# Kernel tuning notes

Hardware: AMD Instinct MI355X
Metric: run time of the kernel (lower is better)

The kernel has to match this reference:

```python
import jax, jax.numpy as jnp
import numpy as np

B, T, N, H, E, R = 512, 10, 50, 200, 10000, 200

def _aggregate(neigh, neigh_len, hist_len, ids, rids, ent, rel, Wa, ba, v):
    # neigh: [B,T,N] entity ids; returns padded GRU input [B,T,3H]
    h = Wa.shape[0]
    e = ent[neigh]                                  # [B,T,N,h] neighbor embeds
    se = ent[ids]                                   # [B,h]
    re_a = ent[rids]                                # faithful: original uses ent_embeds[r] in attention
    Wn, Ws, Wr = Wa[:, :h], Wa[:, h:2 * h], Wa[:, 2 * h:]
    pre = jnp.einsum('btnh,gh->btng', e, Wn) + (se @ Ws.T + re_a @ Wr.T + ba)[:, None, None, :]
    logits = (jnp.tanh(pre) @ v)[..., 0]            # [B,T,N]
    nmask = jnp.arange(neigh.shape[2])[None, None, :] < neigh_len[:, :, None]
    logits = jnp.where(nmask, logits, -1e30)
    w = jax.nn.softmax(logits, axis=-1)             # per-timestep softmax over valid neighbors
    step = jnp.einsum('btn,btnh->bth', w, e)        # attention-pooled neighbor embed
    rr = rel[rids]                                  # rel_embeds used in the GRU-input concat
    seq = jnp.concatenate([step,
                           jnp.broadcast_to(se[:, None, :], step.shape),
                           jnp.broadcast_to(rr[:, None, :], step.shape)], axis=-1)
    smask = jnp.arange(neigh.shape[1])[None, :] < hist_len[:, None]
    return seq * smask[..., None]                   # zeros past each sample's history length

def _gru(seq, lengths, Wih, Whh, bih, bhh):
    # packed_padded GRU equivalent: hidden freezes at each sample's true length
    Bb, Tt, _ = seq.shape
    h = Whh.shape[1]
    mask = jnp.arange(Tt)[None, :] < lengths[:, None]
    def step(hprev, xm):
        x, m = xm
        gi = x @ Wih.T + bih
        gh = hprev @ Whh.T + bhh
        ir, iz, inn = jnp.split(gi, 3, axis=-1)
        hr, hz, hn = jnp.split(gh, 3, axis=-1)
        rg = jax.nn.sigmoid(ir + hr)
        zg = jax.nn.sigmoid(iz + hz)
        ng = jnp.tanh(inn + rg * hn)
        hnew = (1.0 - zg) * ng + zg * hprev
        return jnp.where(m[:, None], hnew, hprev), None
    h0 = jnp.zeros((Bb, h), seq.dtype)
    hf, _ = jax.lax.scan(step, h0, (seq.transpose(1, 0, 2), mask.T))
    return hf

def _ce(logits, labels):
    lp = jax.nn.log_softmax(logits, axis=-1)
    return -jnp.mean(jnp.take_along_axis(lp, labels[:, None], axis=-1)[:, 0])

def setup_inputs() -> dict:
    key = jax.random.key(0)
    ks = jax.random.split(key, 32)
    d = {}
    d['triplets'] = jnp.stack([jax.random.randint(ks[0], (B,), 0, E),
                               jax.random.randint(ks[1], (B,), 0, R),
                               jax.random.randint(ks[2], (B,), 0, E)], axis=1)
    d['s_hist_neigh'] = jax.random.randint(ks[3], (B, T, N), 0, E)
    d['s_neigh_len'] = jax.random.randint(ks[4], (B, T), 1, N + 1)
    d['s_hist_len'] = jax.random.randint(ks[5], (B,), 1, T + 1)
    d['o_hist_neigh'] = jax.random.randint(ks[6], (B, T, N), 0, E)
    d['o_neigh_len'] = jax.random.randint(ks[7], (B, T), 1, N + 1)
    d['o_hist_len'] = jax.random.randint(ks[8], (B,), 1, T + 1)
    sc = 0.05
    d['ent_embeds'] = jax.random.normal(ks[9], (E, H)) * sc
    d['rel_embeds'] = jax.random.normal(ks[10], (R, H)) * sc
    d['attn_s_w'] = jax.random.normal(ks[11], (H, 3 * H)) * sc
    d['attn_s_b'] = jnp.zeros((H,))
    d['v_s'] = jax.random.normal(ks[12], (H, 1)) * sc
    d['attn_o_w'] = jax.random.normal(ks[13], (H, 3 * H)) * sc
    d['attn_o_b'] = jnp.zeros((H,))
    d['v_o'] = jax.random.normal(ks[14], (H, 1)) * sc
    d['sub_w_ih'] = jax.random.normal(ks[15], (3 * H, 3 * H)) * sc
    d['sub_w_hh'] = jax.random.normal(ks[16], (3 * H, H)) * sc
    d['sub_b_ih'] = jnp.zeros((3 * H,))
    d['sub_b_hh'] = jnp.zeros((3 * H,))
    d['ob_w_ih'] = jax.random.normal(ks[17], (3 * H, 3 * H)) * sc
    d['ob_w_hh'] = jax.random.normal(ks[18], (3 * H, H)) * sc
    d['ob_b_ih'] = jnp.zeros((3 * H,))
    d['ob_b_hh'] = jnp.zeros((3 * H,))
    d['lin_sub_w'] = jax.random.normal(ks[19], (E, 3 * H)) * sc
    d['lin_sub_b'] = jnp.zeros((E,))
    d['lin_ob_w'] = jax.random.normal(ks[20], (E, 3 * H)) * sc
    d['lin_ob_b'] = jnp.zeros((E,))
    return d

def reference(triplets, s_hist_neigh, s_neigh_len, s_hist_len, o_hist_neigh, o_neigh_len, o_hist_len,
              ent_embeds, rel_embeds, attn_s_w, attn_s_b, v_s, attn_o_w, attn_o_b, v_o,
              sub_w_ih, sub_w_hh, sub_b_ih, sub_b_hh, ob_w_ih, ob_w_hh, ob_b_ih, ob_b_hh,
              lin_sub_w, lin_sub_b, lin_ob_w, lin_ob_b):
    s, r, o = triplets[:, 0], triplets[:, 1], triplets[:, 2]
    s_idx = jnp.argsort(-s_hist_len)   # descending sort by history length
    o_idx = jnp.argsort(-o_hist_len)
    seq_s = _aggregate(s_hist_neigh, s_neigh_len, s_hist_len, s, r, ent_embeds, rel_embeds, attn_s_w, attn_s_b, v_s)
    seq_o = _aggregate(o_hist_neigh, o_neigh_len, o_hist_len, o, r, ent_embeds, rel_embeds, attn_o_w, attn_o_b, v_o)
    s_h = _gru(seq_s, s_hist_len, sub_w_ih, sub_w_hh, sub_b_ih, sub_b_hh)[s_idx]
    o_h = _gru(seq_o, o_hist_len, ob_w_ih, ob_w_hh, ob_b_ih, ob_b_hh)[o_idx]
    ob_pred = jnp.concatenate([ent_embeds[s[s_idx]], s_h, rel_embeds[r[s_idx]]], axis=1) @ lin_sub_w.T + lin_sub_b
    sub_pred = jnp.concatenate([ent_embeds[o[o_idx]], o_h, rel_embeds[r[o_idx]]], axis=1) @ lin_ob_w.T + lin_ob_b
    loss = _ce(ob_pred, o[s_idx]) + _ce(sub_pred, s[o_idx])
    return loss, sub_pred, ob_pred, o_idx, s_idx
```

## Files before the change

### kernel.cpp

```cpp
#include <hip/hip_runtime.h>
#include <hip/hip_bf16.h>
#include <math.h>

typedef __hip_bfloat16 bf16;
typedef __attribute__((ext_vector_type(8))) short short8;
typedef __attribute__((ext_vector_type(4))) float f32x4;

#define B_ 512
#define T_ 10
#define N_ 50
#define H_ 200
#define E_ 10000
#define R_ 200
#define K3 600

__device__ __forceinline__ float b2f(bf16 x){ return __bfloat162float(x); }
__device__ __forceinline__ float u2f(unsigned short u){
  unsigned int x = ((unsigned int)u) << 16;
  return __builtin_bit_cast(float, x);
}
__device__ __forceinline__ float fsigm(float x){
  return __builtin_amdgcn_rcpf(1.f + __expf(-x));
}
__device__ __forceinline__ float ftanh(float x){
  x = fminf(15.f, fmaxf(-15.f, x));
  float e = __expf(-2.f * x);
  return (1.f - e) * __builtin_amdgcn_rcpf(1.f + e);
}

__global__ void k_init(float* lossacc){ if(threadIdx.x < 4) lossacc[threadIdx.x] = 0.f; }

__global__ __launch_bounds__(256) void k_pack_wn(
    const float* __restrict__ Wa0, const float* __restrict__ Wa1, bf16* __restrict__ Wn2)
{
  int r = blockIdx.x;
  const float* Wa = (r < 200) ? Wa0 : Wa1;
  int g = (r < 200) ? r : r - 200;
  bf16* out = Wn2 + (size_t)r * 256;
  for (int k = threadIdx.x; k < 256; k += 256) {
    float v = (r < 400 && k < 200) ? Wa[(size_t)g * K3 + k] : 0.f;
    out[k] = __float2bfloat16(v);
  }
}

__global__ __launch_bounds__(256) void k_pack_w400(
    const float* __restrict__ W0, const float* __restrict__ W1,
    bf16* __restrict__ dst, int nrows, int rpad)
{
  int r = blockIdx.x, side = blockIdx.y;
  const float* W = side ? W1 : W0;
  bf16* out = dst + ((size_t)side * rpad + r) * 448;
  for (int k = threadIdx.x; k < 448; k += 256) {
    float v = (r < nrows && k < 400) ? W[(size_t)r * K3 + 200 + k] : 0.f;
    out[k] = __float2bfloat16(v);
  }
}

__global__ __launch_bounds__(256) void k_pack_wstep(
    const float* __restrict__ W0, const float* __restrict__ W1, bf16* __restrict__ dst)
{
  int r = blockIdx.x, side = blockIdx.y;
  const float* W = side ? W1 : W0;
  bf16* out = dst + ((size_t)side * 640 + r) * 256;
  for (int k = threadIdx.x; k < 256; k += 256) {
    float v = (r < 600 && k < 200) ? W[(size_t)r * K3 + k] : 0.f;
    out[k] = __float2bfloat16(v);
  }
}

__global__ __launch_bounds__(256) void k_pack_whh(
    const float* __restrict__ W0, const float* __restrict__ W1, bf16* __restrict__ dst)
{
  int r = blockIdx.x, side = blockIdx.y;
  const float* W = side ? W1 : W0;
  bf16* out = dst + ((size_t)side * 608 + r) * 224;
  for (int k = threadIdx.x; k < 224; k += 256) {
    float v = (r < 600 && k < 200) ? W[(size_t)r * H_ + k] : 0.f;
    out[k] = __float2bfloat16(v);
  }
}

__global__ __launch_bounds__(256) void k_afeats(
    const float* __restrict__ ent, const float* __restrict__ rel, const int* __restrict__ trip,
    bf16* __restrict__ Ab, bf16* __restrict__ Ag)
{
  int b = blockIdx.x, side = blockIdx.y;
  int ids = trip[b * 3 + (side ? 2 : 0)];
  int rid = trip[b * 3 + 1];
  size_t ro = ((size_t)side * B_ + b) * 448;
  for (int k = threadIdx.x; k < 448; k += 256) {
    float vb = 0.f, vg = 0.f;
    if (k < 200) { float e = ent[(size_t)ids * H_ + k]; vb = e; vg = e; }
    else if (k < 400) {
      vb = ent[(size_t)rid * H_ + (k - 200)];
      vg = rel[(size_t)rid * H_ + (k - 200)];
    }
    Ab[ro + k] = __float2bfloat16(vb);
    Ag[ro + k] = __float2bfloat16(vg);
  }
}

template<bool OUTBF, bool AF32>
__global__ __launch_bounds__(256) void k_gg(
    const void* __restrict__ Aptr, const bf16* __restrict__ Bptr,
    const float* __restrict__ bias0, const float* __restrict__ bias1,
    void* __restrict__ Cptr,
    int M, int Nout, int KP, int Acols,
    long Astride, long Bstride, long Cstride, int Nstride)
{
  int side = blockIdx.z;
  int m0 = blockIdx.x * 128, n0 = blockIdx.y * 64;

  __shared__ bf16 As[128][72];
  __shared__ bf16 Bs[64][72];

  int tid = threadIdx.x;
  int wave = tid >> 6, lane = tid & 63;
  int quad = lane >> 4, l15 = lane & 15;

  f32x4 acc[8];
  #pragma unroll
  for (int mt = 0; mt < 8; mt++) acc[mt] = (f32x4){0,0,0,0};

  int arow = tid >> 1, ac0 = (tid & 1) * 32;
  int gr = m0 + arow; if (gr > M - 1) gr = M - 1;
  int brow = tid >> 2, bc0 = (tid & 3) * 16;

  for (int k0 = 0; k0 < KP; k0 += 64) {
    if (AF32) {
      const float* src = (const float*)Aptr + (size_t)gr * Acols;
      #pragma unroll
      for (int u = 0; u < 8; u++) {
        int kk = k0 + ac0 + u * 4;
        float4 v;
        if (kk + 4 <= Acols) v = *(const float4*)&src[kk];
        else {
          v.x = (kk + 0 < Acols) ? src[kk + 0] : 0.f;
          v.y = (kk + 1 < Acols) ? src[kk + 1] : 0.f;
          v.z = (kk + 2 < Acols) ? src[kk + 2] : 0.f;
          v.w = (kk + 3 < Acols) ? src[kk + 3] : 0.f;
        }
        As[arow][ac0 + u * 4 + 0] = __float2bfloat16(v.x);
        As[arow][ac0 + u * 4 + 1] = __float2bfloat16(v.y);
        As[arow][ac0 + u * 4 + 2] = __float2bfloat16(v.z);
        As[arow][ac0 + u * 4 + 3] = __float2bfloat16(v.w);
      }
    } else {
      const bf16* src = (const bf16*)Aptr + (size_t)side * Astride + (size_t)gr * KP + k0 + ac0;
      #pragma unroll
      for (int u = 0; u < 4; u++)
        *(short8*)&As[arow][ac0 + u * 8] = *(const short8*)&src[u * 8];
    }
    {
      const bf16* src = Bptr + (size_t)side * Bstride + (size_t)(n0 + brow) * KP + k0 + bc0;
      *(short8*)&Bs[brow][bc0]     = *(const short8*)&src[0];
      *(short8*)&Bs[brow][bc0 + 8] = *(const short8*)&src[8];
    }
    __syncthreads();
    #pragma unroll
    for (int ks = 0; ks < 2; ks++) {
      int kk = ks * 32 + quad * 8;
      short8 bfr = *(const short8*)&Bs[wave * 16 + l15][kk];
      #pragma unroll
      for (int mt = 0; mt < 8; mt++) {
        short8 afr = *(const short8*)&As[mt * 16 + l15][kk];
        acc[mt] = __builtin_amdgcn_mfma_f32_16x16x32_bf16(afr, bfr, acc[mt], 0, 0, 0);
      }
    }
    __syncthreads();
  }

  int n = n0 + wave * 16 + l15;
  if (n < Nout) {
    float bv = bias0 ? (side ? bias1[n] : bias0[n]) : 0.f;
    #pragma unroll
    for (int mt = 0; mt < 8; mt++) {
      #pragma unroll
      for (int r = 0; r < 4; r++) {
        int m = m0 + mt * 16 + quad * 4 + r;
        if (m < M) {
          float val = acc[mt][r] + bv;
          if (OUTBF)
            ((bf16*)Cptr)[(size_t)side * Cstride + (size_t)m * Nstride + n] = __float2bfloat16(val);
          else
            ((float*)Cptr)[(size_t)side * Cstride + (size_t)m * Nstride + n] = val;
        }
      }
    }
  }
}

__global__ __launch_bounds__(256) void k_attn3(
    const float* __restrict__ ent,
    const int* __restrict__ neigh0, const int* __restrict__ neigh1,
    const int* __restrict__ nlen0, const int* __restrict__ nlen1,
    const int* __restrict__ hlen0, const int* __restrict__ hlen1,
    const float* __restrict__ v0, const float* __restrict__ v1,
    const bf16* __restrict__ ep2, const float* __restrict__ biasb,
    bf16* __restrict__ stepb)
{
  int side = blockIdx.y;
  int bt = blockIdx.x;
  int b = bt / T_, t = bt % T_;
  int hl = (side ? hlen1 : hlen0)[b];
  bf16* srow = stepb + (((size_t)side * B_ + b) * T_ + t) * 256;
  int tid = threadIdx.x;
  if (t >= hl) {
    srow[tid] = __float2bfloat16(0.f);
    return;
  }
  const int* neigh = side ? neigh1 : neigh0;
  const float* v = side ? v1 : v0;
  const float* brow = biasb + ((size_t)side * B_ + b) * H_;
  int nl = (side ? nlen1 : nlen0)[b * T_ + t];

  __shared__ float bsh[H_], vsh[H_], lg[64], wsh[64];
  __shared__ int nb[N_];
  if (tid < H_) { bsh[tid] = brow[tid]; vsh[tid] = v[tid]; }
  if (tid < N_) nb[tid] = neigh[((size_t)b * T_ + t) * N_ + tid];
  __syncthreads();

  int grp = tid >> 4;
  int l16 = tid & 15;

  float bs[13], vs[13];
  #pragma unroll
  for (int i = 0; i < 13; i++) {
    int g = l16 + i * 16;
    bool ok = (g < H_);
    bs[i] = ok ? bsh[g] : 0.f;
    vs[i] = ok ? vsh[g] : 0.f;
  }

  for (int n = grp; n < nl; n += 16) {
    const bf16* er = ep2 + (size_t)nb[n] * 400 + side * 200;
    float acc = 0.f;
    #pragma unroll
    for (int i = 0; i < 13; i++) {
      int g = l16 + i * 16;
      float e = (g < H_) ? b2f(er[g]) : 0.f;
      acc += ftanh(e + bs[i]) * vs[i];
    }
    #pragma unroll
    for (int off = 8; off > 0; off >>= 1) acc += __shfl_down(acc, off, 16);
    if (l16 == 0) lg[n] = acc;
  }
  __syncthreads();

  if (tid < 64) {
    float x = (tid < nl) ? lg[tid] : -1e30f;
    float m = x;
    #pragma unroll
    for (int off = 32; off > 0; off >>= 1) m = fmaxf(m, __shfl_down(m, off));
    m = __shfl(m, 0);
    float e = (tid < nl) ? __expf(x - m) : 0.f;
    float s = e;
    #pragma unroll
    for (int off = 32; off > 0; off >>= 1) s += __shfl_down(s, off);
    s = __shfl(s, 0);
    if (tid < N_) wsh[tid] = e / s;
  }
  __syncthreads();

  int h = tid;
  if (h < H_) {
    float a0 = 0.f, a1 = 0.f, a2 = 0.f, a3 = 0.f;
    int n = 0;
    for (; n + 4 <= nl; n += 4) {
      a0 += wsh[n + 0] * ent[(size_t)nb[n + 0] * H_ + h];
      a1 += wsh[n + 1] * ent[(size_t)nb[n + 1] * H_ + h];
      a2 += wsh[n + 2] * ent[(size_t)nb[n + 2] * H_ + h];
      a3 += wsh[n + 3] * ent[(size_t)nb[n + 3] * H_ + h];
    }
    for (; n < nl; n++) a0 += wsh[n] * ent[(size_t)nb[n] * H_ + h];
    srow[h] = __float2bfloat16((a0 + a1) + (a2 + a3));
  } else {
    srow[h] = __float2bfloat16(0.f);
  }
}

__global__ __launch_bounds__(832) void k_gru4(
    const bf16* __restrict__ giall, const bf16* __restrict__ gibase,
    const bf16* __restrict__ Whh2,
    const float* __restrict__ bhh0, const float* __restrict__ bhh1,
    const int* __restrict__ len0, const int* __restrict__ len1,
    float* __restrict__ hfin)
{
  int side = blockIdx.y;
  int b0 = blockIdx.x * 16;
  const bf16* gia = giall + ((size_t)side * B_ * T_ + (size_t)b0 * T_) * 600;
  const bf16* gib = gibase + ((size_t)side * B_ + b0) * K3;
  const bf16* Wh  = Whh2 + (size_t)side * 608 * 224;
  const float* bhh = side ? bhh1 : bhh0;
  const int* len = side ? len1 : len0;

  __shared__ __align__(16) bf16 Hs[2][16][232];

  int tid = threadIdx.x;
  int wave = tid >> 6, lane = tid & 63;
  int quad = lane >> 4, l15 = lane & 15;

  for (int i = tid; i < 2 * 16 * 232 / 8; i += 832) ((short8*)&Hs[0][0][0])[i] = (short8)0;

  int j0 = wave * 16;
  int j = j0 + l15;
  bool jok = (j < H_);
  float bhr = 0.f, bhz = 0.f, bhn = 0.f;
  float gr[4] = {}, gz[4] = {}, gn[4] = {};
  int lens4[4];
  #pragma unroll
  for (int r = 0; r < 4; r++) lens4[r] = len[b0 + quad * 4 + r];
  if (jok) {
    bhr = bhh[j]; bhz = bhh[H_ + j]; bhn = bhh[2 * H_ + j];
    #pragma unroll
    for (int r = 0; r < 4; r++) {
      const bf16* g = gib + (size_t)(quad * 4 + r) * K3;
      gr[r] = b2f(g[j]); gz[r] = b2f(g[H_ + j]); gn[r] = b2f(g[2 * H_ + j]);
    }
  }
  const bf16* wr = Wh + (size_t)j * 224;
  const bf16* wz = Wh + (size_t)(200 + j) * 224;
  const bf16* wn = Wh + (size_t)(400 + j) * 224;
  __syncthreads();

  int cur = 0;
  for (int t = 0; t < T_; t++) {
    unsigned short guR[4], guZ[4], guN[4];
    if (jok) {
      #pragma unroll
      for (int r = 0; r < 4; r++) {
        const unsigned short* g =
            (const unsigned short*)(gia + ((size_t)(quad * 4 + r) * T_ + t) * 600);
        guR[r] = g[j]; guZ[r] = g[200 + j]; guN[r] = g[400 + j];
      }
    }
    f32x4 ar = {0,0,0,0}, az = {0,0,0,0}, anh = {0,0,0,0};
    #pragma unroll
    for (int ks = 0; ks < 7; ks++) {
      int kk = ks * 32 + quad * 8;
      short8 a0 = *(const short8*)&Hs[cur][l15][kk];
      short8 br = *(const short8*)&wr[kk];
      short8 bz = *(const short8*)&wz[kk];
      short8 bn = *(const short8*)&wn[kk];
      ar  = __builtin_amdgcn_mfma_f32_16x16x32_bf16(a0, br, ar, 0, 0, 0);
      az  = __builtin_amdgcn_mfma_f32_16x16x32_bf16(a0, bz, az, 0, 0, 0);
      anh = __builtin_amdgcn_mfma_f32_16x16x32_bf16(a0, bn, anh, 0, 0, 0);
    }
    if (jok) {
      #pragma unroll
      for (int r = 0; r < 4; r++) {
        int row = quad * 4 + r;
        float rz  = ar[r] + u2f(guR[r]) + gr[r] + bhr;
        float zz  = az[r] + u2f(guZ[r]) + gz[r] + bhz;
        float inn = u2f(guN[r]) + gn[r];
        float hn  = anh[r] + bhn;
        float rg = fsigm(rz);
        float zg = fsigm(zz);
        float ng = ftanh(inn + rg * hn);
        float hold = b2f(Hs[cur][row][j]);
        float hnew = (1.f - zg) * ng + zg * hold;
        Hs[cur ^ 1][row][j] = __float2bfloat16((t < lens4[r]) ? hnew : hold);
      }
    }
    __syncthreads();
    cur ^= 1;
  }
  for (int i = tid; i < 16 * H_; i += 832) {
    int row = i / H_, jj = i % H_;
    hfin[((size_t)side * B_ + b0 + row) * H_ + jj] = b2f(Hs[cur][row][jj]);
  }
}

__global__ __launch_bounds__(512) void k_argsort(
    const int* __restrict__ hlen0, const int* __restrict__ hlen1,
    int* __restrict__ idxbuf, float* __restrict__ dout)
{
  int side = blockIdx.x;
  const int* len = side ? hlen1 : hlen0;
  __shared__ int lens[B_];
  __shared__ int perm[B_];
  int tid = threadIdx.x;
  lens[tid] = len[tid];
  __syncthreads();
  int L = lens[tid];
  int rank = 0;
  for (int j = 0; j < B_; j++) {
    int Lj = lens[j];
    rank += (Lj > L) || (Lj == L && j < tid);
  }
  perm[rank] = tid;
  __syncthreads();
  idxbuf[side * B_ + tid] = perm[tid];
  size_t base = 1 + (size_t)2 * B_ * E_ + (side ? 0 : B_);
  dout[base + tid] = (float)perm[tid];
}

__global__ __launch_bounds__(256) void k_feat(
    const float* __restrict__ ent, const float* __restrict__ rel, const int* __restrict__ trip,
    const int* __restrict__ idxbuf, const float* __restrict__ hfin,
    bf16* __restrict__ xfeat)
{
  int i = blockIdx.x, p = blockIdx.y;
  int bi = idxbuf[(p == 0 ? 1 : 0) * B_ + i];
  int ent_id = (p == 0) ? trip[bi * 3 + 2] : trip[bi * 3 + 0];
  int rid = trip[bi * 3 + 1];
  const float* hsrc = hfin + (size_t)(p == 0 ? 1 : 0) * B_ * H_;
  bf16* x = xfeat + ((size_t)p * B_ + i) * 640;
  int h = threadIdx.x;
  if (h < H_) {
    x[h]          = __float2bfloat16(ent[(size_t)ent_id * H_ + h]);
    x[H_ + h]     = __float2bfloat16(hsrc[(size_t)bi * H_ + h]);
    x[2 * H_ + h] = __float2bfloat16(rel[(size_t)rid * H_ + h]);
  }
  if (h < 40) x[600 + h] = __float2bfloat16(0.f);
}

__global__ __launch_bounds__(512) void k_gemm5(
    const bf16* __restrict__ Abf,
    const float* __restrict__ B0, const float* __restrict__ B1,
    const float* __restrict__ bias0, const float* __restrict__ bias1,
    float* __restrict__ dout)
{
  int side = blockIdx.z;
  const float* Bm = side ? B1 : B0;
  const float* bias = side ? bias1 : bias0;
  float* C = dout + 1 + (size_t)side * B_ * E_;
  int mBase = blockIdx.x * 256;
  int m0 = side * B_ + mBase;
  int n0 = blockIdx.y * 64;

  __shared__ bf16 As[256][72];
  __shared__ bf16 Bs[64][72];

  int tid = threadIdx.x;
  int wave = tid >> 6, lane = tid & 63;
  int quad = lane >> 4, l15 = lane & 15;
  int wm = wave >> 1, wn = wave & 1;

  f32x4 acc[4][2];
  #pragma unroll
  for (int mt = 0; mt < 4; mt++)
    #pragma unroll
    for (int nt = 0; nt < 2; nt++) acc[mt][nt] = (f32x4){0,0,0,0};

  int arow = tid >> 1, ac0 = (tid & 1) * 32;
  int brow = tid >> 3, bc0 = (tid & 7) * 8;
  const bf16* asrc = Abf + (size_t)(m0 + arow) * 640 + ac0;
  int nsrc = n0 + brow; if (nsrc > E_ - 1) nsrc = E_ - 1;
  const float* bsrc = Bm + (size_t)nsrc * K3 + bc0;

  for (int k0 = 0; k0 < 640; k0 += 64) {
    #pragma unroll
    for (int u = 0; u < 4; u++)
      *(short8*)&As[arow][ac0 + u * 8] = *(const short8*)&asrc[k0 + u * 8];
    {
      int kb = k0 + bc0;
      if (kb + 8 <= K3) {
        float4 v0 = *(const float4*)&bsrc[k0];
        float4 v1 = *(const float4*)&bsrc[k0 + 4];
        Bs[brow][bc0 + 0] = __float2bfloat16(v0.x);
        Bs[brow][bc0 + 1] = __float2bfloat16(v0.y);
        Bs[brow][bc0 + 2] = __float2bfloat16(v0.z);
        Bs[brow][bc0 + 3] = __float2bfloat16(v0.w);
        Bs[brow][bc0 + 4] = __float2bfloat16(v1.x);
        Bs[brow][bc0 + 5] = __float2bfloat16(v1.y);
        Bs[brow][bc0 + 6] = __float2bfloat16(v1.z);
        Bs[brow][bc0 + 7] = __float2bfloat16(v1.w);
      } else {
        #pragma unroll
        for (int u = 0; u < 8; u++) {
          int k = kb + u;
          float v = (k < K3) ? bsrc[k0 + u] : 0.f;
          Bs[brow][bc0 + u] = __float2bfloat16(v);
        }
      }
    }
    __syncthreads();
    #pragma unroll
    for (int ks = 0; ks < 2; ks++) {
      int kk = ks * 32 + quad * 8;
      short8 bfr[2];
      #pragma unroll
      for (int nt = 0; nt < 2; nt++)
        bfr[nt] = *(const short8*)&Bs[wn * 32 + nt * 16 + l15][kk];
      #pragma unroll
      for (int mt = 0; mt < 4; mt++) {
        short8 afr = *(const short8*)&As[wm * 64 + mt * 16 + l15][kk];
        #pragma unroll
        for (int nt = 0; nt < 2; nt++)
          acc[mt][nt] = __builtin_amdgcn_mfma_f32_16x16x32_bf16(afr, bfr[nt], acc[mt][nt], 0, 0, 0);
      }
    }
    __syncthreads();
  }

  #pragma unroll
  for (int nt = 0; nt < 2; nt++) {
    int n = n0 + wn * 32 + nt * 16 + l15;
    if (n < E_) {
      float bv = bias[n];
      #pragma unroll
      for (int mt = 0; mt < 4; mt++) {
        #pragma unroll
        for (int r = 0; r < 4; r++) {
          int mrow = mBase + wm * 64 + mt * 16 + quad * 4 + r;
          C[(size_t)mrow * E_ + n] = acc[mt][nt][r] + bv;
        }
      }
    }
  }
}

__global__ __launch_bounds__(256) void k_loss(
    const float* __restrict__ dout, const int* __restrict__ trip,
    const int* __restrict__ idxbuf, float* __restrict__ lossacc)
{
  int i = blockIdx.x, p = blockIdx.y;
  const float* row = dout + 1 + (size_t)p * B_ * E_ + (size_t)i * E_;
  int tid = threadIdx.x;
  float m = -1e30f, s = 0.f;
  for (int e = tid; e < E_; e += 256) {
    float x = row[e];
    if (x > m) { s = s * expf(m - x) + 1.f; m = x; }
    else s += expf(x - m);
  }
  __shared__ float ms[256], ss[256];
  ms[tid] = m; ss[tid] = s; __syncthreads();
  for (int st = 128; st > 0; st >>= 1) {
    if (tid < st) {
      float m2 = ms[tid + st], s2 = ss[tid + st];
      float m1 = ms[tid], s1 = ss[tid];
      float mm = fmaxf(m1, m2);
      ss[tid] = s1 * expf(m1 - mm) + s2 * expf(m2 - mm);
      ms[tid] = mm;
    }
    __syncthreads();
  }
  if (tid == 0) {
    int bi = idxbuf[(p == 0 ? 1 : 0) * B_ + i];
    int label = (p == 0) ? trip[bi * 3 + 0] : trip[bi * 3 + 2];
    float lp = row[label] - ms[0] - logf(ss[0]);
    atomicAdd(lossacc, -lp / (float)B_);
  }
}

__global__ void k_loss_write(const float* __restrict__ lossacc, float* __restrict__ dout){
  if (threadIdx.x == 0) dout[0] = lossacc[0];
}

extern "C" void kernel_launch(void* const* d_in, const int* in_sizes, int n_in,
                              void* d_out, int out_size, void* d_ws, size_t ws_size,
                              hipStream_t stream)
{
  const int* trip = (const int*)d_in[0];
  const int* s_ne = (const int*)d_in[1];
  const int* s_nl = (const int*)d_in[2];
  const int* s_hl = (const int*)d_in[3];
  const int* o_ne = (const int*)d_in[4];
  const int* o_nl = (const int*)d_in[5];
  const int* o_hl = (const int*)d_in[6];
  const float* ent = (const float*)d_in[7];
  const float* rel = (const float*)d_in[8];
  const float* aw_s = (const float*)d_in[9];
  const float* ab_s = (const float*)d_in[10];
  const float* v_s  = (const float*)d_in[11];
  const float* aw_o = (const float*)d_in[12];
  const float* ab_o = (const float*)d_in[13];
  const float* v_o  = (const float*)d_in[14];
  const float* sub_wih = (const float*)d_in[15];
  const float* sub_whh = (const float*)d_in[16];
  const float* sub_bih = (const float*)d_in[17];
  const float* sub_bhh = (const float*)d_in[18];
  const float* ob_wih  = (const float*)d_in[19];
  const float* ob_whh  = (const float*)d_in[20];
  const float* ob_bih  = (const float*)d_in[21];
  const float* ob_bhh  = (const float*)d_in[22];
  const float* lin_sub_w = (const float*)d_in[23];
  const float* lin_sub_b = (const float*)d_in[24];
  const float* lin_ob_w  = (const float*)d_in[25];
  const float* lin_ob_b  = (const float*)d_in[26];
  float* dout = (float*)d_out;

  char* w = (char*)d_ws;
  bf16* ep2     = (bf16*)w;  w += (size_t)E_ * 400 * 2;
  bf16* stepb   = (bf16*)w;  w += (size_t)2 * B_ * T_ * 256 * 2;
  float* biasb  = (float*)w; w += (size_t)2 * B_ * H_ * 4;
  bf16* gibase  = (bf16*)w;  w += (size_t)2 * B_ * K3 * 2;
  float* hfin   = (float*)w; w += (size_t)2 * B_ * H_ * 4;
  bf16* xfeat   = (bf16*)w;  w += (size_t)1024 * 640 * 2;
  bf16* Wn2     = (bf16*)w;  w += (size_t)448 * 256 * 2;
  bf16* Wb2     = (bf16*)w;  w += (size_t)2 * 256 * 448 * 2;
  bf16* Wg2     = (bf16*)w;  w += (size_t)2 * 640 * 448 * 2;
  bf16* Wstep   = (bf16*)w;  w += (size_t)2 * 640 * 256 * 2;
  bf16* Whh2    = (bf16*)w;  w += (size_t)2 * 608 * 224 * 2;
  bf16* giall   = (bf16*)w;  w += (size_t)2 * B_ * T_ * 600 * 2;
  bf16* Abias   = (bf16*)w;  w += (size_t)2 * B_ * 448 * 2;
  bf16* Agi     = (bf16*)w;  w += (size_t)2 * B_ * 448 * 2;
  float* lossacc= (float*)w; w += 256;
  int* idxbuf   = (int*)w;   w += 4096;

  k_init<<<1, 64, 0, stream>>>(lossacc);
  k_pack_wn<<<448, 256, 0, stream>>>(aw_s, aw_o, Wn2);
  k_pack_w400<<<dim3(256, 2), 256, 0, stream>>>(aw_s, aw_o, Wb2, 200, 256);
  k_pack_w400<<<dim3(640, 2), 256, 0, stream>>>(sub_wih, ob_wih, Wg2, 600, 640);
  k_pack_wstep<<<dim3(640, 2), 256, 0, stream>>>(sub_wih, ob_wih, Wstep);
  k_pack_whh<<<dim3(608, 2), 256, 0, stream>>>(sub_whh, ob_whh, Whh2);
  k_afeats<<<dim3(B_, 2), 256, 0, stream>>>(ent, rel, trip, Abias, Agi);
  k_gg<true, true><<<dim3(79, 7, 1), 256, 0, stream>>>(
      (const void*)ent, Wn2, nullptr, nullptr, (void*)ep2,
      E_, 400, 256, 200, 0L, 0L, 0L, 400);
  k_gg<false, false><<<dim3(4, 4, 2), 256, 0, stream>>>(
      (const void*)Abias, Wb2, ab_s, ab_o, (void*)biasb,
      B_, 200, 448, 448, (long)B_ * 448, 256L * 448, (long)B_ * 200, 200);
  k_gg<true, false><<<dim3(4, 10, 2), 256, 0, stream>>>(
      (const void*)Agi, Wg2, sub_bih, ob_bih, (void*)gibase,
      B_, 600, 448, 448, (long)B_ * 448, 640L * 448, (long)B_ * 600, 600);
  k_attn3<<<dim3(B_ * T_, 2), 256, 0, stream>>>(ent, s_ne, o_ne, s_nl, o_nl,
                                                s_hl, o_hl, v_s, v_o, ep2, biasb, stepb);
  k_gg<true, false><<<dim3(40, 10, 2), 256, 0, stream>>>(
      (const void*)stepb, Wstep, nullptr, nullptr, (void*)giall,
      B_ * T_, 600, 256, 256, (long)B_ * T_ * 256, 640L * 256, (long)B_ * T_ * 600, 600);
  k_gru4<<<dim3(B_ / 16, 2), 832, 0, stream>>>(giall, gibase, Whh2, sub_bhh, ob_bhh,
                                               s_hl, o_hl, hfin);
  k_argsort<<<2, 512, 0, stream>>>(s_hl, o_hl, idxbuf, dout);
  k_feat<<<dim3(B_, 2), 256, 0, stream>>>(ent, rel, trip, idxbuf, hfin, xfeat);
  k_gemm5<<<dim3(2, (E_ + 63) / 64, 2), 512, 0, stream>>>(
      xfeat, lin_ob_w, lin_sub_w, lin_ob_b, lin_sub_b, dout);
  k_loss<<<dim3(B_, 2), 256, 0, stream>>>(dout, trip, idxbuf, lossacc);
  k_loss_write<<<1, 64, 0, stream>>>(lossacc, dout);
}
```

Baseline: 421.0 us.

## Pre-pack output linear weights to bf16 and merge pack kernels into one launch

Merges the six small packing and init kernels into a single launch, which cuts launch overhead. Adds a kernel that converts the two 10000x600 fp32 output-projection weights into padded bf16 once per call. A new GEMM then reads these bf16 tiles directly instead of converting fp32 to bf16 inside every tile load. The cost is an extra full pass over about 48MB of fp32 weights plus a bf16 write, and the new path only runs if the workspace is large enough.

```diff
diff --git a/kernel.cpp b/kernel.cpp
--- a/kernel.cpp
+++ b/kernel.cpp
@@ -13,6 +13,7 @@
 #define E_ 10000
 #define R_ 200
 #define K3 600
+#define EP_ 10048
 
 __device__ __forceinline__ float b2f(bf16 x){ return __bfloat162float(x); }
 __device__ __forceinline__ float u2f(unsigned short u){
@@ -28,75 +29,93 @@
   return (1.f - e) * __builtin_amdgcn_rcpf(1.f + e);
 }
 
-__global__ void k_init(float* lossacc){ if(threadIdx.x < 4) lossacc[threadIdx.x] = 0.f; }
-
-__global__ __launch_bounds__(256) void k_pack_wn(
-    const float* __restrict__ Wa0, const float* __restrict__ Wa1, bf16* __restrict__ Wn2)
-{
-  int r = blockIdx.x;
-  const float* Wa = (r < 200) ? Wa0 : Wa1;
-  int g = (r < 200) ? r : r - 200;
-  bf16* out = Wn2 + (size_t)r * 256;
-  for (int k = threadIdx.x; k < 256; k += 256) {
-    float v = (r < 400 && k < 200) ? Wa[(size_t)g * K3 + k] : 0.f;
+__global__ __launch_bounds__(256) void k_packall(
+    const float* __restrict__ aw_s, const float* __restrict__ aw_o,
+    const float* __restrict__ sub_wih, const float* __restrict__ ob_wih,
+    const float* __restrict__ sub_whh, const float* __restrict__ ob_whh,
+    const float* __restrict__ ent, const float* __restrict__ rel,
+    const int* __restrict__ trip,
+    bf16* __restrict__ Wn2, bf16* __restrict__ Wb2, bf16* __restrict__ Wg2,
+    bf16* __restrict__ Wstep, bf16* __restrict__ Whh2,
+    bf16* __restrict__ Ab, bf16* __restrict__ Ag, float* __restrict__ lossacc)
+{
+  int bid = blockIdx.x;
+  int tid = threadIdx.x;
+  if (bid < 448) {
+    int r = bid;
+    const float* Wa = (r < 200) ? aw_s : aw_o;
+    int g = (r < 200) ? r : r - 200;
+    bf16* out = Wn2 + (size_t)r * 256;
+    for (int k = tid; k < 256; k += 256) {
+      float v = (r < 400 && k < 200) ? Wa[(size_t)g * K3 + k] : 0.f;
+      out[k] = __float2bfloat16(v);
+    }
+  } else if (bid < 960) {
+    int idx = bid - 448;
+    int side = idx >> 8, r = idx & 255;
+    const float* W = side ? aw_o : aw_s;
+    bf16* out = Wb2 + ((size_t)side * 256 + r) * 448;
+    for (int k = tid; k < 448; k += 256) {
+      float v = (r < 200 && k < 400) ? W[(size_t)r * K3 + 200 + k] : 0.f;
+      out[k] = __float2bfloat16(v);
+    }
+  } else if (bid < 2240) {
+    int idx = bid - 960;
+    int side = idx / 640, r = idx % 640;
+    const float* W = side ? ob_wih : sub_wih;
+    bf16* out = Wg2 + ((size_t)side * 640 + r) * 448;
+    for (int k = tid; k < 448; k += 256) {
+      float v = (r < 600 && k < 400) ? W[(size_t)r * K3 + 200 + k] : 0.f;
+      out[k] = __float2bfloat16(v);
+    }
+  } else if (bid < 3520) {
+    int idx = bid - 2240;
+    int side = idx / 640, r = idx % 640;
+    const float* W = side ? ob_wih : sub_wih;
+    bf16* out = Wstep + ((size_t)side * 640 + r) * 256;
+    for (int k = tid; k < 256; k += 256) {
+      float v = (r < 600 && k < 200) ? W[(size_t)r * K3 + k] : 0.f;
+      out[k] = __float2bfloat16(v);
+    }
+  } else if (bid < 4736) {
+    int idx = bid - 3520;
+    int side = idx / 608, r = idx % 608;
+    const float* W = side ? ob_whh : sub_whh;
+    bf16* out = Whh2 + ((size_t)side * 608 + r) * 224;
+    for (int k = tid; k < 224; k += 256) {
+      float v = (r < 600 && k < 200) ? W[(size_t)r * H_ + k] : 0.f;
+      out[k] = __float2bfloat16(v);
+    }
+  } else if (bid < 5760) {
+    int idx = bid - 4736;
+    int side = idx >> 9, b = idx & 511;
+    int ids = trip[b * 3 + (side ? 2 : 0)];
+    int rid = trip[b * 3 + 1];
+    size_t ro = ((size_t)side * B_ + b) * 448;
+    for (int k = tid; k < 448; k += 256) {
+      float vb = 0.f, vg = 0.f;
+      if (k < 200) { float e = ent[(size_t)ids * H_ + k]; vb = e; vg = e; }
+      else if (k < 400) {
+        vb = ent[(size_t)rid * H_ + (k - 200)];
+        vg = rel[(size_t)rid * H_ + (k - 200)];
+      }
+      Ab[ro + k] = __float2bfloat16(vb);
+      Ag[ro + k] = __float2bfloat16(vg);
+    }
+  } else {
+    if (tid < 4) lossacc[tid] = 0.f;
+  }
+}
+
+__global__ __launch_bounds__(256) void k_pack_lin(
+    const float* __restrict__ W0, const float* __restrict__ W1, bf16* __restrict__ Wlin)
+{
+  int row = blockIdx.x, side = blockIdx.y;
+  const float* W = side ? W1 : W0;
+  bf16* out = Wlin + ((size_t)side * EP_ + row) * 640;
+  for (int k = threadIdx.x; k < 640; k += 256) {
+    float v = (row < E_ && k < K3) ? W[(size_t)row * K3 + k] : 0.f;
     out[k] = __float2bfloat16(v);
-  }
-}
-
-__global__ __launch_bounds__(256) void k_pack_w400(
-    const float* __restrict__ W0, const float* __restrict__ W1,
-    bf16* __restrict__ dst, int nrows, int rpad)
-{
-  int r = blockIdx.x, side = blockIdx.y;
-  const float* W = side ? W1 : W0;
-  bf16* out = dst + ((size_t)side * rpad + r) * 448;
-  for (int k = threadIdx.x; k < 448; k += 256) {
-    float v = (r < nrows && k < 400) ? W[(size_t)r * K3 + 200 + k] : 0.f;
-    out[k] = __float2bfloat16(v);
-  }
-}
-
-__global__ __launch_bounds__(256) void k_pack_wstep(
-    const float* __restrict__ W0, const float* __restrict__ W1, bf16* __restrict__ dst)
-{
-  int r = blockIdx.x, side = blockIdx.y;
-  const float* W = side ? W1 : W0;
-  bf16* out = dst + ((size_t)side * 640 + r) * 256;
-  for (int k = threadIdx.x; k < 256; k += 256) {
-    float v = (r < 600 && k < 200) ? W[(size_t)r * K3 + k] : 0.f;
-    out[k] = __float2bfloat16(v);
-  }
-}
-
-__global__ __launch_bounds__(256) void k_pack_whh(
-    const float* __restrict__ W0, const float* __restrict__ W1, bf16* __restrict__ dst)
-{
-  int r = blockIdx.x, side = blockIdx.y;
-  const float* W = side ? W1 : W0;
-  bf16* out = dst + ((size_t)side * 608 + r) * 224;
-  for (int k = threadIdx.x; k < 224; k += 256) {
-    float v = (r < 600 && k < 200) ? W[(size_t)r * H_ + k] : 0.f;
-    out[k] = __float2bfloat16(v);
-  }
-}
-
-__global__ __launch_bounds__(256) void k_afeats(
-    const float* __restrict__ ent, const float* __restrict__ rel, const int* __restrict__ trip,
-    bf16* __restrict__ Ab, bf16* __restrict__ Ag)
-{
-  int b = blockIdx.x, side = blockIdx.y;
-  int ids = trip[b * 3 + (side ? 2 : 0)];
-  int rid = trip[b * 3 + 1];
-  size_t ro = ((size_t)side * B_ + b) * 448;
-  for (int k = threadIdx.x; k < 448; k += 256) {
-    float vb = 0.f, vg = 0.f;
-    if (k < 200) { float e = ent[(size_t)ids * H_ + k]; vb = e; vg = e; }
-    else if (k < 400) {
-      vb = ent[(size_t)rid * H_ + (k - 200)];
-      vg = rel[(size_t)rid * H_ + (k - 200)];
-    }
-    Ab[ro + k] = __float2bfloat16(vb);
-    Ag[ro + k] = __float2bfloat16(vg);
   }
 }
 
@@ -413,6 +432,79 @@
     x[2 * H_ + h] = __float2bfloat16(rel[(size_t)rid * H_ + h]);
   }
   if (h < 40) x[600 + h] = __float2bfloat16(0.f);
+}
+
+__global__ __launch_bounds__(512) void k_gemm6(
+    const bf16* __restrict__ Abf, const bf16* __restrict__ Wlin,
+    const float* __restrict__ bias0, const float* __restrict__ bias1,
+    float* __restrict__ dout)
+{
+  int side = blockIdx.z;
+  const bf16* Bm = Wlin + (size_t)side * EP_ * 640;
+  const float* bias = side ? bias1 : bias0;
+  float* C = dout + 1 + (size_t)side * B_ * E_;
+  int mBase = blockIdx.x * 256;
+  int m0 = side * B_ + mBase;
+  int n0 = blockIdx.y * 64;
+
+  __shared__ bf16 As[256][72];
+  __shared__ bf16 Bs[64][72];
+
+  int tid = threadIdx.x;
+  int wave = tid >> 6, lane = tid & 63;
+  int quad = lane >> 4, l15 = lane & 15;
+  int wm = wave >> 1, wn = wave & 1;
+
+  f32x4 acc[4][2];
+  #pragma unroll
+  for (int mt = 0; mt < 4; mt++)
+    #pragma unroll
+    for (int nt = 0; nt < 2; nt++) acc[mt][nt] = (f32x4){0,0,0,0};
+
+  int arow = tid >> 1, ac0 = (tid & 1) * 32;
+  int brow = tid >> 3, bc0 = (tid & 7) * 8;
+  const bf16* asrc = Abf + (size_t)(m0 + arow) * 640 + ac0;
+  const bf16* bsrc = Bm + (size_t)(n0 + brow) * 640 + bc0;
+
+  for (int k0 = 0; k0 < 640; k0 += 64) {
+    #pragma unroll
+    for (int u = 0; u < 4; u++)
+      *(short8*)&As[arow][ac0 + u * 8] = *(const short8*)&asrc[k0 + u * 8];
+    *(short8*)&Bs[brow][bc0] = *(const short8*)&bsrc[k0];
+    __syncthreads();
+    #pragma unroll
+    for (int ks = 0; ks < 2; ks++) {
+      int kk = ks * 32 + quad * 8;
+      short8 bfr[2];
+      #pragma unroll
+      for (int nt = 0; nt < 2; nt++)
+        bfr[nt] = *(const short8*)&Bs[wn * 32 + nt * 16 + l15][kk];
+      #pragma unroll
+      for (int mt = 0; mt < 4; mt++) {
+        short8 afr = *(const short8*)&As[wm * 64 + mt * 16 + l15][kk];
+        #pragma unroll
+        for (int nt = 0; nt < 2; nt++)
+          acc[mt][nt] = __builtin_amdgcn_mfma_f32_16x16x32_bf16(afr, bfr[nt], acc[mt][nt], 0, 0, 0);
+      }
+    }
+    __syncthreads();
+  }
+
+  #pragma unroll
+  for (int nt = 0; nt < 2; nt++) {
+    int n = n0 + wn * 32 + nt * 16 + l15;
+    if (n < E_) {
+      float bv = bias[n];
+      #pragma unroll
+      for (int mt = 0; mt < 4; mt++) {
+        #pragma unroll
+        for (int r = 0; r < 4; r++) {
+          int mrow = mBase + wm * 64 + mt * 16 + quad * 4 + r;
+          C[(size_t)mrow * E_ + n] = acc[mt][nt][r] + bv;
+        }
+      }
+    }
+  }
 }
 
 __global__ __launch_bounds__(512) void k_gemm5(
@@ -598,14 +690,14 @@
   bf16* Agi     = (bf16*)w;  w += (size_t)2 * B_ * 448 * 2;
   float* lossacc= (float*)w; w += 256;
   int* idxbuf   = (int*)w;   w += 4096;
-
-  k_init<<<1, 64, 0, stream>>>(lossacc);
-  k_pack_wn<<<448, 256, 0, stream>>>(aw_s, aw_o, Wn2);
-  k_pack_w400<<<dim3(256, 2), 256, 0, stream>>>(aw_s, aw_o, Wb2, 200, 256);
-  k_pack_w400<<<dim3(640, 2), 256, 0, stream>>>(sub_wih, ob_wih, Wg2, 600, 640);
-  k_pack_wstep<<<dim3(640, 2), 256, 0, stream>>>(sub_wih, ob_wih, Wstep);
-  k_pack_whh<<<dim3(608, 2), 256, 0, stream>>>(sub_whh, ob_whh, Whh2);
-  k_afeats<<<dim3(B_, 2), 256, 0, stream>>>(ent, rel, trip, Abias, Agi);
+  bf16* Wlin    = (bf16*)w;  w += (size_t)2 * EP_ * 640 * 2;
+  bool useBf16B = ((size_t)(w - (char*)d_ws) <= ws_size);
+
+  k_packall<<<5761, 256, 0, stream>>>(aw_s, aw_o, sub_wih, ob_wih, sub_whh, ob_whh,
+                                      ent, rel, trip, Wn2, Wb2, Wg2, Wstep, Whh2,
+                                      Abias, Agi, lossacc);
+  if (useBf16B)
+    k_pack_lin<<<dim3(EP_, 2), 256, 0, stream>>>(lin_ob_w, lin_sub_w, Wlin);
   k_gg<true, true><<<dim3(79, 7, 1), 256, 0, stream>>>(
       (const void*)ent, Wn2, nullptr, nullptr, (void*)ep2,
       E_, 400, 256, 200, 0L, 0L, 0L, 400);
@@ -624,8 +716,12 @@
                                                s_hl, o_hl, hfin);
   k_argsort<<<2, 512, 0, stream>>>(s_hl, o_hl, idxbuf, dout);
   k_feat<<<dim3(B_, 2), 256, 0, stream>>>(ent, rel, trip, idxbuf, hfin, xfeat);
-  k_gemm5<<<dim3(2, (E_ + 63) / 64, 2), 512, 0, stream>>>(
-      xfeat, lin_ob_w, lin_sub_w, lin_ob_b, lin_sub_b, dout);
+  if (useBf16B)
+    k_gemm6<<<dim3(2, (E_ + 63) / 64, 2), 512, 0, stream>>>(
+        xfeat, Wlin, lin_ob_b, lin_sub_b, dout);
+  else
+    k_gemm5<<<dim3(2, (E_ + 63) / 64, 2), 512, 0, stream>>>(
+        xfeat, lin_ob_w, lin_sub_w, lin_ob_b, lin_sub_b, dout);
   k_loss<<<dim3(B_, 2), 256, 0, stream>>>(dout, trip, idxbuf, lossacc);
   k_loss_write<<<1, 64, 0, stream>>>(lossacc, dout);
 }
```

Result: faster. 409.5 us (-2.7%).
